# Kernel tuning notes

Hardware: AMD Instinct MI355X
Metric: run time of the kernel (lower is better)

Reference implementation:

```python
import jax, jax.numpy as jnp
import numpy as np
import math

B, T, C = 2, 2048, 1024
H = 16
HD = C // H  # 64
LAMBDA_INIT = 0.7 - 0.6 * math.exp(-0.3 * (2 - 1))
EPS = 1e-5


def setup_inputs() -> dict:
    key = jax.random.key(0)
    ks = jax.random.split(key, 12)
    s = 1.0 / math.sqrt(C)
    return {
        'x':   jax.random.normal(ks[0], (B, T, C), jnp.float32),
        'Wq1': jax.random.normal(ks[1], (C, C), jnp.float32) * s,
        'Wq2': jax.random.normal(ks[2], (C, C), jnp.float32) * s,
        'Wk1': jax.random.normal(ks[3], (C, C), jnp.float32) * s,
        'Wk2': jax.random.normal(ks[4], (C, C), jnp.float32) * s,
        'Wv':  jax.random.normal(ks[5], (2 * C, C), jnp.float32) * s,
        'Wc':  jax.random.normal(ks[6], (C, 2 * C), jnp.float32) * (1.0 / math.sqrt(2 * C)),
        'lq1': jax.random.normal(ks[7], (H, HD), jnp.float32) * 0.1,
        'lk1': jax.random.normal(ks[8], (H, HD), jnp.float32) * 0.1,
        'lq2': jax.random.normal(ks[9], (H, HD), jnp.float32) * 0.1,
        'lk2': jax.random.normal(ks[10], (H, HD), jnp.float32) * 0.1,
    }


def _heads(x, W, d):
    # x:[B,T,C] @ W.T:[C,out] -> [B,H,T,d]
    b, t, _ = x.shape
    return jnp.einsum('btc,dc->btd', x, W).reshape(b, t, H, d).transpose(0, 2, 1, 3)


def reference(x, Wq1, Wq2, Wk1, Wk2, Wv, Wc, lq1, lk1, lq2, lk2):
    b, t, c = x.shape
    q1 = _heads(x, Wq1, HD)
    q2 = _heads(x, Wq2, HD)
    k1 = _heads(x, Wk1, HD)
    k2 = _heads(x, Wk2, HD)
    v = _heads(x, Wv, 2 * HD)  # [B,H,T,2hd]
    scale = 1.0 / math.sqrt(HD)
    causal = jnp.tril(jnp.ones((t, t), bool))  # [T,T]
    neg = jnp.float32(-jnp.inf)
    att1 = jnp.einsum('bhqd,bhkd->bhqk', q1, k1) * scale
    att2 = jnp.einsum('bhqd,bhkd->bhqk', q2, k2) * scale
    att1 = jax.nn.softmax(jnp.where(causal, att1, neg), axis=-1)
    att2 = jax.nn.softmax(jnp.where(causal, att2, neg), axis=-1)
    lam1 = jnp.exp(jnp.sum(lq1 * lk1, -1))  # [H]
    lam2 = jnp.exp(jnp.sum(lq2 * lk2, -1))
    lam_full = (lam1 - lam2 + LAMBDA_INIT)[None, :, None, None]
    att = att1 - lam_full * att2
    y = jnp.einsum('bhqk,bhkd->bhqd', att, v)  # [B,H,T,2hd]
    # sub-layernorm over last dim, no affine
    mu = jnp.mean(y, -1, keepdims=True)
    var = jnp.mean(jnp.square(y - mu), -1, keepdims=True)
    y = (y - mu) * jax.lax.rsqrt(var + EPS)
    y = y * (1.0 - LAMBDA_INIT)
    y = y.transpose(0, 2, 1, 3).reshape(b, t, 2 * c)
    return jnp.einsum('btd,cd->btc', y, Wc)
```

## Files before the change

### kernel.cpp

```cpp
#include <hip/hip_runtime.h>
#include <stdint.h>

typedef unsigned short u16;
typedef unsigned int   u32;
typedef short  short8  __attribute__((ext_vector_type(8)));
typedef float  f32x4   __attribute__((ext_vector_type(4)));
typedef u16    u16x4   __attribute__((ext_vector_type(4)));
typedef u32    u32x4   __attribute__((ext_vector_type(4)));

#define LAMBDA_INIT   0.25550906759096927f
#define ONE_MINUS_LI  0.7444909324090307f
#define QSCALE        0.18033688011112043f

__device__ __forceinline__ u16 f2bf(float f) {
  union { float f; u32 u; } v; v.f = f;
  u32 r = v.u + 0x7fffu + ((v.u >> 16) & 1u);
  return (u16)(r >> 16);
}

__device__ __forceinline__ u32 packtr(float a, float b) {
  return (__builtin_bit_cast(u32, a) >> 16) | (__builtin_bit_cast(u32, b) & 0xffff0000u);
}

__device__ __forceinline__ float expv(float x) {
  float r; asm("v_exp_f32 %0, %1" : "=v"(r) : "v"(x)); return r;
}

__device__ __forceinline__ void gload16(const void* g, void* l) {
  __builtin_amdgcn_global_load_lds(
      (const __attribute__((address_space(1))) void*)g,
      (__attribute__((address_space(3))) void*)l, 16, 0, 0);
}

__global__ __launch_bounds__(256) void k_cvt12(
    const float* __restrict__ x,  const float* __restrict__ wq1,
    const float* __restrict__ wq2, const float* __restrict__ wk1,
    const float* __restrict__ wk2, const float* __restrict__ wv,
    const float* __restrict__ wc,
    u16* __restrict__ xb, u16* __restrict__ wall, u16* __restrict__ wcb) {
  const int seg = blockIdx.y;
  const float* s;
  u16* d;
  if (seg < 4)       { s = x + (size_t)seg * 1048576;        d = xb + (size_t)seg * 1048576; }
  else if (seg == 4) { s = wq1;                              d = wall; }
  else if (seg == 5) { s = wq2;                              d = wall + 1048576; }
  else if (seg == 6) { s = wk1;                              d = wall + 2097152; }
  else if (seg == 7) { s = wk2;                              d = wall + 3145728; }
  else if (seg < 10) { s = wv + (size_t)(seg - 8) * 1048576; d = wall + 4194304 + (size_t)(seg - 8) * 1048576; }
  else               { s = wc + (size_t)(seg - 10) * 1048576; d = wcb + (size_t)(seg - 10) * 1048576; }
  int i = (blockIdx.x * 256 + threadIdx.x) * 4;
  float4 v = *(const float4*)(s + i);
  u16x4 o = { f2bf(v.x), f2bf(v.y), f2bf(v.z), f2bf(v.w) };
  *(u16x4*)(d + i) = o;
}

__device__ __forceinline__ void gemm_tile_128(
    const u16* __restrict__ A, const u16* __restrict__ Bm, int K,
    int m0, int n0, char* smem, f32x4 acc[4][4]) {
  const int tid = threadIdx.x;
  const int l = tid & 63, w = tid >> 6, g = l >> 4, q = l & 15;
  const int wm = w >> 1, wn = w & 1;
  char* As = smem;
  char* Bs = smem + 16384;
#pragma unroll
  for (int mi = 0; mi < 4; mi++)
#pragma unroll
    for (int ni = 0; ni < 4; ni++) acc[mi][ni] = (f32x4){0.f, 0.f, 0.f, 0.f};

  const int nkt = K >> 6;
  for (int kt = 0; kt < nkt; ++kt) {
    __syncthreads();
#pragma unroll
    for (int i = 0; i < 4; i++) {
      int cc = i * 256 + tid;
      int row = cc >> 3, off = cc & 7;
      int sw = (off * 16) ^ ((row & 7) << 4);
      gload16((const char*)A + ((size_t)(m0 + row) * K + kt * 64) * 2 + sw, As + cc * 16);
      gload16((const char*)Bm + ((size_t)(n0 + row) * K + kt * 64) * 2 + sw, Bs + cc * 16);
    }
    __syncthreads();
#pragma unroll
    for (int ks = 0; ks < 2; ++ks) {
      short8 af[4], bf[4];
#pragma unroll
      for (int mi = 0; mi < 4; mi++) {
        int row = wm * 64 + mi * 16 + q;
        af[mi] = *(const short8*)(As + ((row * 128 + ks * 64 + g * 16) ^ ((row & 7) << 4)));
      }
#pragma unroll
      for (int ni = 0; ni < 4; ni++) {
        int row = wn * 64 + ni * 16 + q;
        bf[ni] = *(const short8*)(Bs + ((row * 128 + ks * 64 + g * 16) ^ ((row & 7) << 4)));
      }
#pragma unroll
      for (int mi = 0; mi < 4; mi++)
#pragma unroll
        for (int ni = 0; ni < 4; ni++)
          acc[mi][ni] = __builtin_amdgcn_mfma_f32_16x16x32_bf16(af[mi], bf[ni], acc[mi][ni], 0, 0, 0);
    }
  }
}

__global__ __launch_bounds__(256) void k_gemm_qkv(
    const u16* __restrict__ xb, const u16* __restrict__ wall,
    u16* __restrict__ q1, u16* __restrict__ q2,
    u16* __restrict__ k1, u16* __restrict__ k2,
    u16* __restrict__ vt) {
  __shared__ __align__(16) char smem[32768];
  f32x4 acc[4][4];
  const int n0 = blockIdx.x * 128, m0 = blockIdx.y * 128;
  gemm_tile_128(xb, wall, 1024, m0, n0, smem, acc);

  const int l = threadIdx.x & 63, w = threadIdx.x >> 6, g = l >> 4, q = l & 15;
  const int wm = w >> 1, wn = w & 1;
  const int seg = n0 >> 10;
  const float sc = (seg < 2) ? QSCALE : 1.0f;
  u16* qk = (seg == 0) ? q1 : (seg == 1) ? q2 : (seg == 2) ? k1 : k2;
#pragma unroll
  for (int mi = 0; mi < 4; mi++)
#pragma unroll
    for (int ni = 0; ni < 4; ni++) {
      int row0 = m0 + wm * 64 + mi * 16 + 4 * g;
      int col = n0 + wn * 64 + ni * 16 + q;
      int bb = row0 >> 11;
      if (seg < 4) {
        int h = (col >> 6) & 15, hd = col & 63;
#pragma unroll
        for (int r = 0; r < 4; r++) {
          int t = (row0 + r) & 2047;
          qk[(((size_t)bb * 16 + h) * 2048 + t) * 64 + hd] = f2bf(acc[mi][ni][r] * sc);
        }
      } else {
        int nv = col - 4096, hh = nv >> 7, d = nv & 127;
        int t = row0 & 2047;
        u16x4 pv;
#pragma unroll
        for (int r = 0; r < 4; r++) pv[r] = f2bf(acc[mi][ni][r]);
        size_t addr = (size_t)(bb * 16 + hh) * 262144 + (size_t)(t >> 6) * 8192
                    + (size_t)(((((t >> 5) & 1) * 8 + (d >> 4)) * 512)
                               + ((t >> 3) & 3) * 128 + (d & 15) * 8 + (t & 7));
        *(u16x4*)(vt + addr) = pv;
      }
    }
}

__global__ __launch_bounds__(256) void k_attn(
    const u16* __restrict__ q1p, const u16* __restrict__ q2p,
    const u16* __restrict__ k1p, const u16* __restrict__ k2p,
    const u16* __restrict__ vfp,
    const float* __restrict__ lq1, const float* __restrict__ lk1,
    const float* __restrict__ lq2, const float* __restrict__ lk2,
    u16* __restrict__ ybp) {
  __shared__ __align__(16) char smem[65536];
  const int fid = blockIdx.x;
  const int bh = (fid & 7) * 4 + (fid >> 7);
  const int xA = (fid >> 3) & 15;
  const int b = bh >> 4, h = bh & 15;
  const int tid = threadIdx.x, w = tid >> 6, l = tid & 63, g = l >> 4, q = l & 15;
  const int nA = xA + 1;

  float a1 = lq1[h * 64 + l] * lk1[h * 64 + l];
  float a2 = lq2[h * 64 + l] * lk2[h * 64 + l];
#pragma unroll
  for (int off = 32; off; off >>= 1) {
    a1 += __shfl_xor(a1, off);
    a2 += __shfl_xor(a2, off);
  }
  const float lam = expf(a1) - expf(a2) + LAMBDA_INIT;

  short8 qf[2][2];
  f32x4 o[2][8];
  float lsum[2];
  int qrow = 0;

  auto init_tile = [&](int q0) {
    qrow = q0 + w * 16 + q;
    size_t qoff = ((size_t)bh * 2048 + qrow) * 64;
#pragma unroll
    for (int ks = 0; ks < 2; ++ks) {
      qf[0][ks] = *(const short8*)(q1p + qoff + ks * 32 + g * 8);
      qf[1][ks] = *(const short8*)(q2p + qoff + ks * 32 + g * 8);
    }
#pragma unroll
    for (int s = 0; s < 2; s++) {
      lsum[s] = 0.f;
#pragma unroll
      for (int mt = 0; mt < 8; mt++) o[s][mt] = (f32x4){0.f, 0.f, 0.f, 0.f};
    }
  };

  auto stage_kv = [&](char* sb, int kv0) {
#pragma unroll
    for (int i = 0; i < 2; i++) {
      int cc = i * 256 + tid, kv = cc >> 3, off = cc & 7;
      int sw = (off * 16) ^ ((kv & 7) << 4);
      size_t rb = ((size_t)bh * 2048 + kv0 + kv) * 128;
      gload16((const char*)k1p + rb + sw, sb + cc * 16);
      gload16((const char*)k2p + rb + sw, sb + 8192 + cc * 16);
    }
    const char* vsrc = (const char*)vfp + (size_t)bh * 524288 + (size_t)(kv0 >> 6) * 16384;
#pragma unroll
    for (int i = 0; i < 4; i++) {
      int cc = i * 256 + tid;
      gload16(vsrc + cc * 16, sb + 16384 + cc * 16);
    }
  };

  auto epilogue = [&]() {
    float l0 = lsum[0]; l0 += __shfl_xor(l0, 16); l0 += __shfl_xor(l0, 32);
    float l1 = lsum[1]; l1 += __shfl_xor(l1, 16); l1 += __shfl_xor(l1, 32);
    const float inv0 = 1.f / l0, inv1 = 1.f / l1;
    float sum = 0.f, ssq = 0.f;
#pragma unroll
    for (int mt = 0; mt < 8; ++mt)
#pragma unroll
      for (int r = 0; r < 4; r++) {
        float y = o[0][mt][r] * inv0 - lam * (o[1][mt][r] * inv1);
        o[0][mt][r] = y;
        sum += y;
        ssq += y * y;
      }
    sum += __shfl_xor(sum, 16); sum += __shfl_xor(sum, 32);
    ssq += __shfl_xor(ssq, 16); ssq += __shfl_xor(ssq, 32);
    const float mean = sum * (1.f / 128.f);
    const float var = ssq * (1.f / 128.f) - mean * mean;
    const float rstd = rsqrtf(var + 1e-5f) * ONE_MINUS_LI;
    u16* dst = ybp + ((size_t)(b * 2048 + qrow)) * 2048 + h * 128;
#pragma unroll
    for (int mt = 0; mt < 8; ++mt) {
      u16x4 pv;
#pragma unroll
      for (int r = 0; r < 4; r++) pv[r] = f2bf((o[0][mt][r] - mean) * rstd);
      *(u16x4*)(dst + mt * 16 + 4 * g) = pv;
    }
  };

  init_tile(xA * 64);
  stage_kv(smem, 0);

  for (int i = 0; i < 33; ++i) {
    char* sb = smem + (i & 1) * 32768;
    asm volatile("s_waitcnt vmcnt(0)" ::: "memory");
    __builtin_amdgcn_s_barrier();
    if (i + 1 < 33) {
      int kvn = (i + 1 < nA) ? (i + 1) * 64 : (i + 1 - nA) * 64;
      stage_kv(smem + ((i + 1) & 1) * 32768, kvn);
    }

    const int kv0 = (i < nA) ? i * 64 : (i - nA) * 64;
    const bool diag = (i == nA - 1) || (i == 32);

#pragma unroll
    for (int kk = 0; kk < 2; ++kk) {
      u32 pk[2][4];
#pragma unroll
      for (int s = 0; s < 2; ++s) {
        const char* Ks = sb + s * 8192;
        f32x4 s0 = {0.f, 0.f, 0.f, 0.f}, s1 = {0.f, 0.f, 0.f, 0.f};
#pragma unroll
        for (int ks = 0; ks < 2; ++ks) {
          short8 af0 = *(const short8*)(Ks + (((kk * 32 + q) * 128 + ks * 64 + g * 16) ^ ((q & 7) << 4)));
          short8 af1 = *(const short8*)(Ks + (((kk * 32 + 16 + q) * 128 + ks * 64 + g * 16) ^ ((q & 7) << 4)));
          s0 = __builtin_amdgcn_mfma_f32_16x16x32_bf16(af0, qf[s][ks], s0, 0, 0, 0);
          s1 = __builtin_amdgcn_mfma_f32_16x16x32_bf16(af1, qf[s][ks], s1, 0, 0, 0);
        }
        const int kb0 = kv0 + kk * 32 + 4 * g, kb1 = kb0 + 16;
        if (diag) {
#pragma unroll
          for (int r = 0; r < 4; r++) {
            s0[r] = (kb0 + r > qrow) ? -1e30f : s0[r];
            s1[r] = (kb1 + r > qrow) ? -1e30f : s1[r];
          }
        }
        float p0[4], p1[4], rs = 0.f;
#pragma unroll
        for (int r = 0; r < 4; r++) {
          p0[r] = expv(s0[r]);
          p1[r] = expv(s1[r]);
          rs += p0[r] + p1[r];
        }
        lsum[s] += rs;

        u32 pk0[2] = { packtr(p0[0], p0[1]), packtr(p0[2], p0[3]) };
        u32 pk1[2] = { packtr(p1[0], p1[1]), packtr(p1[2], p1[3]) };
        int srcA = q + (g & 1) * 32;
        int srcB = srcA + 16;
        u32 xa0 = (u32)__shfl((int)pk0[0], srcA), xa1 = (u32)__shfl((int)pk0[1], srcA);
        u32 xa2 = (u32)__shfl((int)pk0[0], srcB), xa3 = (u32)__shfl((int)pk0[1], srcB);
        u32 xb0 = (u32)__shfl((int)pk1[0], srcA), xb1 = (u32)__shfl((int)pk1[1], srcA);
        u32 xb2 = (u32)__shfl((int)pk1[0], srcB), xb3 = (u32)__shfl((int)pk1[1], srcB);
        bool lo = (g < 2);
        pk[s][0] = lo ? xa0 : xb0;
        pk[s][1] = lo ? xa1 : xb1;
        pk[s][2] = lo ? xa2 : xb2;
        pk[s][3] = lo ? xa3 : xb3;
      }
      u32x4 t0 = {pk[0][0], pk[0][1], pk[0][2], pk[0][3]};
      u32x4 t1 = {pk[1][0], pk[1][1], pk[1][2], pk[1][3]};
      short8 pf0 = __builtin_bit_cast(short8, t0);
      short8 pf1 = __builtin_bit_cast(short8, t1);
      const char* Vb = sb + 16384 + kk * 8192 + l * 16;
#pragma unroll
      for (int mt = 0; mt < 8; ++mt) {
        short8 vf = *(const short8*)(Vb + mt * 1024);
        o[0][mt] = __builtin_amdgcn_mfma_f32_16x16x32_bf16(vf, pf0, o[0][mt], 0, 0, 0);
        o[1][mt] = __builtin_amdgcn_mfma_f32_16x16x32_bf16(vf, pf1, o[1][mt], 0, 0, 0);
      }
    }

    if (i == nA - 1) {
      epilogue();
      init_tile((31 - xA) * 64);
    }
  }
  epilogue();
}

__global__ __launch_bounds__(512) void k_gemm_out(
    const u16* __restrict__ yb, const u16* __restrict__ wcb,
    float* __restrict__ out) {
  __shared__ __align__(16) char smem[32768];
  const int tid = threadIdx.x;
  const int l = tid & 63, w = tid >> 6, g = l >> 4, q = l & 15;
  const int wm = w >> 1, wn = w & 1;
  const int n0 = blockIdx.x * 128, m0 = blockIdx.y * 128;
  char* As = smem;
  char* Bs = smem + 16384;
  f32x4 acc[2][4];
#pragma unroll
  for (int mi = 0; mi < 2; mi++)
#pragma unroll
    for (int ni = 0; ni < 4; ni++) acc[mi][ni] = (f32x4){0.f, 0.f, 0.f, 0.f};

  for (int kt = 0; kt < 32; ++kt) {
    __syncthreads();
#pragma unroll
    for (int i = 0; i < 2; i++) {
      int cc = i * 512 + tid;
      int row = cc >> 3, off = cc & 7;
      int sw = (off * 16) ^ ((row & 7) << 4);
      gload16((const char*)yb + ((size_t)(m0 + row) * 2048 + kt * 64) * 2 + sw, As + cc * 16);
      gload16((const char*)wcb + ((size_t)(n0 + row) * 2048 + kt * 64) * 2 + sw, Bs + cc * 16);
    }
    __syncthreads();
#pragma unroll
    for (int ks = 0; ks < 2; ++ks) {
      short8 af[2], bf[4];
#pragma unroll
      for (int mi = 0; mi < 2; mi++) {
        int row = wm * 32 + mi * 16 + q;
        af[mi] = *(const short8*)(As + ((row * 128 + ks * 64 + g * 16) ^ ((row & 7) << 4)));
      }
#pragma unroll
      for (int ni = 0; ni < 4; ni++) {
        int row = wn * 64 + ni * 16 + q;
        bf[ni] = *(const short8*)(Bs + ((row * 128 + ks * 64 + g * 16) ^ ((row & 7) << 4)));
      }
#pragma unroll
      for (int mi = 0; mi < 2; mi++)
#pragma unroll
        for (int ni = 0; ni < 4; ni++)
          acc[mi][ni] = __builtin_amdgcn_mfma_f32_16x16x32_bf16(af[mi], bf[ni], acc[mi][ni], 0, 0, 0);
    }
  }
#pragma unroll
  for (int mi = 0; mi < 2; mi++)
#pragma unroll
    for (int ni = 0; ni < 4; ni++)
#pragma unroll
      for (int r = 0; r < 4; r++) {
        int row = m0 + wm * 32 + mi * 16 + 4 * g + r;
        int col = n0 + wn * 64 + ni * 16 + q;
        out[(size_t)row * 1024 + col] = acc[mi][ni][r];
      }
}

extern "C" void kernel_launch(void* const* d_in, const int* in_sizes, int n_in,
                              void* d_out, int out_size, void* d_ws, size_t ws_size,
                              hipStream_t stream) {
  const float* x   = (const float*)d_in[0];
  const float* Wq1 = (const float*)d_in[1];
  const float* Wq2 = (const float*)d_in[2];
  const float* Wk1 = (const float*)d_in[3];
  const float* Wk2 = (const float*)d_in[4];
  const float* Wv  = (const float*)d_in[5];
  const float* Wc  = (const float*)d_in[6];
  const float* lq1 = (const float*)d_in[7];
  const float* lk1 = (const float*)d_in[8];
  const float* lq2 = (const float*)d_in[9];
  const float* lk2 = (const float*)d_in[10];

  char* ws = (char*)d_ws;
  u16* xb   = (u16*)(ws);
  u16* wall = (u16*)(ws + 8388608);
  u16* wcb  = (u16*)(ws + 20971520);
  u16* q1   = (u16*)(ws + 25165824);
  u16* q2   = (u16*)(ws + 33554432);
  u16* k1   = (u16*)(ws + 41943040);
  u16* k2   = (u16*)(ws + 50331648);
  u16* vt   = (u16*)(ws + 58720256);
  u16* yb   = (u16*)(ws + 75497472);

  k_cvt12<<<dim3(1024, 12), 256, 0, stream>>>(x, Wq1, Wq2, Wk1, Wk2, Wv, Wc,
                                              xb, wall, wcb);
  k_gemm_qkv<<<dim3(48, 32), 256, 0, stream>>>(xb, wall, q1, q2, k1, k2, vt);
  k_attn<<<512, 256, 0, stream>>>(q1, q2, k1, k2, vt,
                                  lq1, lk1, lq2, lk2, yb);
  k_gemm_out<<<dim3(8, 32), 512, 0, stream>>>(yb, wcb, (float*)d_out);
}
```

Measured before the change: 208.1 us.

## Replace paired causal tiles with one tile per block and 32-key chunks

The attention kernel stops pairing a short and a long causal query tile in one block. It now launches one block per 64-row query tile, ordered longest first, and walks the keys in 32-key chunks with a 32KB double buffer instead of 64KB. Halving the shared memory should allow more resident blocks per CU, and the longest-first order is meant to keep the load balanced. In exchange there are more barriers and loop iterations per key processed and twice as many blocks.

New measurement: 197.0 us. 1.06x faster.

```diff
diff --git a/kernel.cpp b/kernel.cpp
--- a/kernel.cpp
+++ b/kernel.cpp
@@ -151,13 +151,15 @@
     const float* __restrict__ lq1, const float* __restrict__ lk1,
     const float* __restrict__ lq2, const float* __restrict__ lk2,
     u16* __restrict__ ybp) {
-  __shared__ __align__(16) char smem[65536];
+  __shared__ __align__(16) char smem[32768];
   const int fid = blockIdx.x;
-  const int bh = (fid & 7) * 4 + (fid >> 7);
-  const int xA = (fid >> 3) & 15;
+  const int r9 = fid >> 3;
+  const int tile = 31 - (r9 >> 2);
+  const int bh = (fid & 7) * 4 + (r9 & 3);
   const int b = bh >> 4, h = bh & 15;
   const int tid = threadIdx.x, w = tid >> 6, l = tid & 63, g = l >> 4, q = l & 15;
-  const int nA = xA + 1;
+  const int nchunk = 2 * tile + 2;
+  const int qrow = tile * 64 + w * 16 + q;
 
   float a1 = lq1[h * 64 + l] * lk1[h * 64 + l];
   float a2 = lq2[h * 64 + l] * lk2[h * 64 + l];
@@ -169,151 +171,126 @@
   const float lam = expf(a1) - expf(a2) + LAMBDA_INIT;
 
   short8 qf[2][2];
-  f32x4 o[2][8];
-  float lsum[2];
-  int qrow = 0;
-
-  auto init_tile = [&](int q0) {
-    qrow = q0 + w * 16 + q;
+  {
     size_t qoff = ((size_t)bh * 2048 + qrow) * 64;
 #pragma unroll
     for (int ks = 0; ks < 2; ++ks) {
       qf[0][ks] = *(const short8*)(q1p + qoff + ks * 32 + g * 8);
       qf[1][ks] = *(const short8*)(q2p + qoff + ks * 32 + g * 8);
     }
-#pragma unroll
-    for (int s = 0; s < 2; s++) {
-      lsum[s] = 0.f;
-#pragma unroll
-      for (int mt = 0; mt < 8; mt++) o[s][mt] = (f32x4){0.f, 0.f, 0.f, 0.f};
-    }
+  }
+  f32x4 o[2][8];
+  float lsum[2] = {0.f, 0.f};
+#pragma unroll
+  for (int s = 0; s < 2; s++)
+#pragma unroll
+    for (int mt = 0; mt < 8; mt++) o[s][mt] = (f32x4){0.f, 0.f, 0.f, 0.f};
+
+  auto stage_kv = [&](char* sb, int kv0) {
+    int kv = tid >> 3, off = tid & 7;
+    int sw = (off * 16) ^ ((kv & 7) << 4);
+    size_t rb = ((size_t)bh * 2048 + kv0 + kv) * 128;
+    gload16((const char*)k1p + rb + sw, sb + tid * 16);
+    gload16((const char*)k2p + rb + sw, sb + 4096 + tid * 16);
+    const char* vsrc = (const char*)vfp + (size_t)bh * 524288
+                     + (size_t)(kv0 >> 6) * 16384 + (size_t)((kv0 >> 5) & 1) * 8192;
+    gload16(vsrc + tid * 16, sb + 8192 + tid * 16);
+    gload16(vsrc + 4096 + tid * 16, sb + 12288 + tid * 16);
   };
 
-  auto stage_kv = [&](char* sb, int kv0) {
-#pragma unroll
-    for (int i = 0; i < 2; i++) {
-      int cc = i * 256 + tid, kv = cc >> 3, off = cc & 7;
-      int sw = (off * 16) ^ ((kv & 7) << 4);
-      size_t rb = ((size_t)bh * 2048 + kv0 + kv) * 128;
-      gload16((const char*)k1p + rb + sw, sb + cc * 16);
-      gload16((const char*)k2p + rb + sw, sb + 8192 + cc * 16);
-    }
-    const char* vsrc = (const char*)vfp + (size_t)bh * 524288 + (size_t)(kv0 >> 6) * 16384;
-#pragma unroll
-    for (int i = 0; i < 4; i++) {
-      int cc = i * 256 + tid;
-      gload16(vsrc + cc * 16, sb + 16384 + cc * 16);
-    }
-  };
-
-  auto epilogue = [&]() {
-    float l0 = lsum[0]; l0 += __shfl_xor(l0, 16); l0 += __shfl_xor(l0, 32);
-    float l1 = lsum[1]; l1 += __shfl_xor(l1, 16); l1 += __shfl_xor(l1, 32);
-    const float inv0 = 1.f / l0, inv1 = 1.f / l1;
-    float sum = 0.f, ssq = 0.f;
-#pragma unroll
-    for (int mt = 0; mt < 8; ++mt)
-#pragma unroll
-      for (int r = 0; r < 4; r++) {
-        float y = o[0][mt][r] * inv0 - lam * (o[1][mt][r] * inv1);
-        o[0][mt][r] = y;
-        sum += y;
-        ssq += y * y;
-      }
-    sum += __shfl_xor(sum, 16); sum += __shfl_xor(sum, 32);
-    ssq += __shfl_xor(ssq, 16); ssq += __shfl_xor(ssq, 32);
-    const float mean = sum * (1.f / 128.f);
-    const float var = ssq * (1.f / 128.f) - mean * mean;
-    const float rstd = rsqrtf(var + 1e-5f) * ONE_MINUS_LI;
-    u16* dst = ybp + ((size_t)(b * 2048 + qrow)) * 2048 + h * 128;
-#pragma unroll
-    for (int mt = 0; mt < 8; ++mt) {
-      u16x4 pv;
-#pragma unroll
-      for (int r = 0; r < 4; r++) pv[r] = f2bf((o[0][mt][r] - mean) * rstd);
-      *(u16x4*)(dst + mt * 16 + 4 * g) = pv;
-    }
-  };
-
-  init_tile(xA * 64);
   stage_kv(smem, 0);
 
-  for (int i = 0; i < 33; ++i) {
-    char* sb = smem + (i & 1) * 32768;
+  for (int i = 0; i < nchunk; ++i) {
+    char* sb = smem + (i & 1) * 16384;
     asm volatile("s_waitcnt vmcnt(0)" ::: "memory");
     __builtin_amdgcn_s_barrier();
-    if (i + 1 < 33) {
-      int kvn = (i + 1 < nA) ? (i + 1) * 64 : (i + 1 - nA) * 64;
-      stage_kv(smem + ((i + 1) & 1) * 32768, kvn);
-    }
-
-    const int kv0 = (i < nA) ? i * 64 : (i - nA) * 64;
-    const bool diag = (i == nA - 1) || (i == 32);
-
-#pragma unroll
-    for (int kk = 0; kk < 2; ++kk) {
-      u32 pk[2][4];
-#pragma unroll
-      for (int s = 0; s < 2; ++s) {
-        const char* Ks = sb + s * 8192;
-        f32x4 s0 = {0.f, 0.f, 0.f, 0.f}, s1 = {0.f, 0.f, 0.f, 0.f};
-#pragma unroll
-        for (int ks = 0; ks < 2; ++ks) {
-          short8 af0 = *(const short8*)(Ks + (((kk * 32 + q) * 128 + ks * 64 + g * 16) ^ ((q & 7) << 4)));
-          short8 af1 = *(const short8*)(Ks + (((kk * 32 + 16 + q) * 128 + ks * 64 + g * 16) ^ ((q & 7) << 4)));
-          s0 = __builtin_amdgcn_mfma_f32_16x16x32_bf16(af0, qf[s][ks], s0, 0, 0, 0);
-          s1 = __builtin_amdgcn_mfma_f32_16x16x32_bf16(af1, qf[s][ks], s1, 0, 0, 0);
+    if (i + 1 < nchunk) stage_kv(smem + ((i + 1) & 1) * 16384, (i + 1) * 32);
+
+    const int kv0 = i * 32;
+    const bool diag = (i >= nchunk - 2);
+
+    u32 pk[2][4];
+#pragma unroll
+    for (int s = 0; s < 2; ++s) {
+      const char* Ks = sb + s * 4096;
+      f32x4 s0 = {0.f, 0.f, 0.f, 0.f}, s1 = {0.f, 0.f, 0.f, 0.f};
+#pragma unroll
+      for (int ks = 0; ks < 2; ++ks) {
+        short8 af0 = *(const short8*)(Ks + ((q * 128 + ks * 64 + g * 16) ^ ((q & 7) << 4)));
+        short8 af1 = *(const short8*)(Ks + (((16 + q) * 128 + ks * 64 + g * 16) ^ ((q & 7) << 4)));
+        s0 = __builtin_amdgcn_mfma_f32_16x16x32_bf16(af0, qf[s][ks], s0, 0, 0, 0);
+        s1 = __builtin_amdgcn_mfma_f32_16x16x32_bf16(af1, qf[s][ks], s1, 0, 0, 0);
+      }
+      const int kb0 = kv0 + 4 * g, kb1 = kb0 + 16;
+      if (diag) {
+#pragma unroll
+        for (int r = 0; r < 4; r++) {
+          s0[r] = (kb0 + r > qrow) ? -1e30f : s0[r];
+          s1[r] = (kb1 + r > qrow) ? -1e30f : s1[r];
         }
-        const int kb0 = kv0 + kk * 32 + 4 * g, kb1 = kb0 + 16;
-        if (diag) {
-#pragma unroll
-          for (int r = 0; r < 4; r++) {
-            s0[r] = (kb0 + r > qrow) ? -1e30f : s0[r];
-            s1[r] = (kb1 + r > qrow) ? -1e30f : s1[r];
-          }
-        }
-        float p0[4], p1[4], rs = 0.f;
-#pragma unroll
-        for (int r = 0; r < 4; r++) {
-          p0[r] = expv(s0[r]);
-          p1[r] = expv(s1[r]);
-          rs += p0[r] + p1[r];
-        }
-        lsum[s] += rs;
-
-        u32 pk0[2] = { packtr(p0[0], p0[1]), packtr(p0[2], p0[3]) };
-        u32 pk1[2] = { packtr(p1[0], p1[1]), packtr(p1[2], p1[3]) };
-        int srcA = q + (g & 1) * 32;
-        int srcB = srcA + 16;
-        u32 xa0 = (u32)__shfl((int)pk0[0], srcA), xa1 = (u32)__shfl((int)pk0[1], srcA);
-        u32 xa2 = (u32)__shfl((int)pk0[0], srcB), xa3 = (u32)__shfl((int)pk0[1], srcB);
-        u32 xb0 = (u32)__shfl((int)pk1[0], srcA), xb1 = (u32)__shfl((int)pk1[1], srcA);
-        u32 xb2 = (u32)__shfl((int)pk1[0], srcB), xb3 = (u32)__shfl((int)pk1[1], srcB);
-        bool lo = (g < 2);
-        pk[s][0] = lo ? xa0 : xb0;
-        pk[s][1] = lo ? xa1 : xb1;
-        pk[s][2] = lo ? xa2 : xb2;
-        pk[s][3] = lo ? xa3 : xb3;
-      }
-      u32x4 t0 = {pk[0][0], pk[0][1], pk[0][2], pk[0][3]};
-      u32x4 t1 = {pk[1][0], pk[1][1], pk[1][2], pk[1][3]};
-      short8 pf0 = __builtin_bit_cast(short8, t0);
-      short8 pf1 = __builtin_bit_cast(short8, t1);
-      const char* Vb = sb + 16384 + kk * 8192 + l * 16;
-#pragma unroll
-      for (int mt = 0; mt < 8; ++mt) {
-        short8 vf = *(const short8*)(Vb + mt * 1024);
-        o[0][mt] = __builtin_amdgcn_mfma_f32_16x16x32_bf16(vf, pf0, o[0][mt], 0, 0, 0);
-        o[1][mt] = __builtin_amdgcn_mfma_f32_16x16x32_bf16(vf, pf1, o[1][mt], 0, 0, 0);
-      }
-    }
-
-    if (i == nA - 1) {
-      epilogue();
-      init_tile((31 - xA) * 64);
-    }
-  }
-  epilogue();
+      }
+      float p0[4], p1[4], rs = 0.f;
+#pragma unroll
+      for (int r = 0; r < 4; r++) {
+        p0[r] = expv(s0[r]);
+        p1[r] = expv(s1[r]);
+        rs += p0[r] + p1[r];
+      }
+      lsum[s] += rs;
+
+      u32 pk0[2] = { packtr(p0[0], p0[1]), packtr(p0[2], p0[3]) };
+      u32 pk1[2] = { packtr(p1[0], p1[1]), packtr(p1[2], p1[3]) };
+      int srcA = q + (g & 1) * 32;
+      int srcB = srcA + 16;
+      u32 xa0 = (u32)__shfl((int)pk0[0], srcA), xa1 = (u32)__shfl((int)pk0[1], srcA);
+      u32 xa2 = (u32)__shfl((int)pk0[0], srcB), xa3 = (u32)__shfl((int)pk0[1], srcB);
+      u32 xb0 = (u32)__shfl((int)pk1[0], srcA), xb1 = (u32)__shfl((int)pk1[1], srcA);
+      u32 xb2 = (u32)__shfl((int)pk1[0], srcB), xb3 = (u32)__shfl((int)pk1[1], srcB);
+      bool lo = (g < 2);
+      pk[s][0] = lo ? xa0 : xb0;
+      pk[s][1] = lo ? xa1 : xb1;
+      pk[s][2] = lo ? xa2 : xb2;
+      pk[s][3] = lo ? xa3 : xb3;
+    }
+    u32x4 t0 = {pk[0][0], pk[0][1], pk[0][2], pk[0][3]};
+    u32x4 t1 = {pk[1][0], pk[1][1], pk[1][2], pk[1][3]};
+    short8 pf0 = __builtin_bit_cast(short8, t0);
+    short8 pf1 = __builtin_bit_cast(short8, t1);
+    const char* Vb = sb + 8192 + l * 16;
+#pragma unroll
+    for (int mt = 0; mt < 8; ++mt) {
+      short8 vf = *(const short8*)(Vb + mt * 1024);
+      o[0][mt] = __builtin_amdgcn_mfma_f32_16x16x32_bf16(vf, pf0, o[0][mt], 0, 0, 0);
+      o[1][mt] = __builtin_amdgcn_mfma_f32_16x16x32_bf16(vf, pf1, o[1][mt], 0, 0, 0);
+    }
+  }
+
+  float l0 = lsum[0]; l0 += __shfl_xor(l0, 16); l0 += __shfl_xor(l0, 32);
+  float l1 = lsum[1]; l1 += __shfl_xor(l1, 16); l1 += __shfl_xor(l1, 32);
+  const float inv0 = 1.f / l0, inv1 = 1.f / l1;
+  float sum = 0.f, ssq = 0.f;
+#pragma unroll
+  for (int mt = 0; mt < 8; ++mt)
+#pragma unroll
+    for (int r = 0; r < 4; r++) {
+      float y = o[0][mt][r] * inv0 - lam * (o[1][mt][r] * inv1);
+      o[0][mt][r] = y;
+      sum += y;
+      ssq += y * y;
+    }
+  sum += __shfl_xor(sum, 16); sum += __shfl_xor(sum, 32);
+  ssq += __shfl_xor(ssq, 16); ssq += __shfl_xor(ssq, 32);
+  const float mean = sum * (1.f / 128.f);
+  const float var = ssq * (1.f / 128.f) - mean * mean;
+  const float rstd = rsqrtf(var + 1e-5f) * ONE_MINUS_LI;
+  u16* dst = ybp + ((size_t)(b * 2048 + qrow)) * 2048 + h * 128;
+#pragma unroll
+  for (int mt = 0; mt < 8; ++mt) {
+    u16x4 pv;
+#pragma unroll
+    for (int r = 0; r < 4; r++) pv[r] = f2bf((o[0][mt][r] - mean) * rstd);
+    *(u16x4*)(dst + mt * 16 + 4 * g) = pv;
+  }
 }
 
 __global__ __launch_bounds__(512) void k_gemm_out(
@@ -404,7 +381,7 @@
   k_cvt12<<<dim3(1024, 12), 256, 0, stream>>>(x, Wq1, Wq2, Wk1, Wk2, Wv, Wc,
                                               xb, wall, wcb);
   k_gemm_qkv<<<dim3(48, 32), 256, 0, stream>>>(xb, wall, q1, q2, k1, k2, vt);
-  k_attn<<<512, 256, 0, stream>>>(q1, q2, k1, k2, vt,
-                                  lq1, lk1, lq2, lk2, yb);
+  k_attn<<<1024, 256, 0, stream>>>(q1, q2, k1, k2, vt,
+                                   lq1, lk1, lq2, lk2, yb);
   k_gemm_out<<<dim3(8, 32), 512, 0, stream>>>(yb, wcb, (float*)d_out);
 }
```
